# Kernel tuning notes

Hardware: AMD Instinct MI355X
Metric: run time of the kernel (lower is better)

The kernel has to match this reference:

```python
import jax, jax.numpy as jnp
import numpy as np

B, S, H, E, I, TOP_K = 2, 1024, 1024, 8, 1408, 2
W_SCALE = 0.02


def setup_inputs() -> dict:
    key = jax.random.key(0)
    ks = jax.random.split(key, 5)
    return {
        "hidden_states": jax.random.normal(ks[0], (B, S, H), dtype=jnp.float32),
        "router_weight": jax.random.normal(ks[1], (H, E), dtype=jnp.float32) * W_SCALE,
        "gate_proj": jax.random.normal(ks[2], (E, H, I), dtype=jnp.float32) * W_SCALE,
        "up_proj": jax.random.normal(ks[3], (E, H, I), dtype=jnp.float32) * W_SCALE,
        "down_proj": jax.random.normal(ks[4], (E, I, H), dtype=jnp.float32) * W_SCALE,
        "gate_bias": jnp.zeros((E, I), dtype=jnp.float32),
        "up_bias": jnp.zeros((E, I), dtype=jnp.float32),
        "down_bias": jnp.zeros((E, H), dtype=jnp.float32),
        "top_k": TOP_K,
    }


def reference(hidden_states, router_weight, gate_proj, up_proj, down_proj,
              gate_bias, up_bias, down_bias, top_k):
    b, s, h = hidden_states.shape
    e = gate_proj.shape[0]
    x = hidden_states.reshape(-1, h)              # [T, H], T = b*s
    t = x.shape[0]

    # --- RouterAdapter: MoEGate top-k then scatter into dense scores [T, E] ---
    logits = x @ router_weight                    # [T, E]
    probs = jax.nn.softmax(logits, axis=-1)
    topk_w, topk_idx = jax.lax.top_k(probs, top_k)  # [T, k]
    topk_w = topk_w / jnp.sum(topk_w, axis=-1, keepdims=True)  # norm_topk_prob
    scores = jnp.zeros((t, e), dtype=topk_w.dtype)
    scores = scores.at[jnp.arange(t)[:, None], topk_idx].set(topk_w)

    # --- StackedExperts.sparse_forward (dense equivalent of sparse matmuls) ---
    g = jnp.einsum('th,ehi->tei', x, gate_proj) + gate_bias[None]  # [T, E, I]
    u = jnp.einsum('th,ehi->tei', x, up_proj) + up_bias[None]      # [T, E, I]
    act = jax.nn.silu(g) * u                       # ACTIVATION_DEEPSEEK
    d = jnp.einsum('tei,eih->teh', act, down_proj) + down_bias[None]  # [T, E, H]

    # combine per-expert outputs with router scores (non-routed scores are 0,
    # matching the sparse matmul's zero blocks)
    y = jnp.einsum('teh,te->th', d, scores)
    return y.reshape(b, s, h)
```

## Files before the change

kernel.cpp:

```cpp
#include <hip/hip_runtime.h>

#define T_TOK 2048
#define HDIM  1024
#define NEXP  8
#define IDIM  1408

#define BM 128
#define BN 64
#define BK 32
#define KPAD 40
#define MT_SLOTS 16
#define GU_NT 22
#define DN_NT 16
#define DK_HALF 704

#define GU_BLOCKS   (8 * GU_NT * MT_SLOTS)
#define PREP_RTR    512
#define PREP_GRID   (PREP_RTR + 16 * 176)
#define GUWD_GRID   (GU_BLOCKS + 8 * 176)

typedef __attribute__((ext_vector_type(8))) short bf16x8;
typedef __attribute__((ext_vector_type(4))) float f32x4;

static __device__ __forceinline__ unsigned short f2bf(float f) {
    union { float f; unsigned u; } a; a.f = f;
    return (unsigned short)((a.u + 0x7fffu + ((a.u >> 16) & 1u)) >> 16);
}

__global__ __launch_bounds__(256) void prep_kernel(
    const float* __restrict__ x,
    const float* __restrict__ rw,
    const float* __restrict__ gw,
    const float* __restrict__ uw,
    int*   __restrict__ sel,
    float* __restrict__ w1arr,
    unsigned short* __restrict__ xb,
    unsigned short* __restrict__ gwt,
    unsigned short* __restrict__ uwt)
{
    __shared__ __align__(16) char smem[32768];
    const int tid = threadIdx.x;
    const int bx  = blockIdx.x;

    if (bx < PREP_RTR) {
        float (*rwT)[HDIM] = (float (*)[HDIM])smem;
#pragma unroll
        for (int p = 0; p < 4; ++p) {
            const int h = tid + 256 * p;
            const float4 a = *(const float4*)(rw + (size_t)h * 8);
            const float4 b = *(const float4*)(rw + (size_t)h * 8 + 4);
            rwT[0][h] = a.x; rwT[1][h] = a.y; rwT[2][h] = a.z; rwT[3][h] = a.w;
            rwT[4][h] = b.x; rwT[5][h] = b.y; rwT[6][h] = b.z; rwT[7][h] = b.w;
        }
        __syncthreads();

        const int t    = bx * 4 + (tid >> 6);
        const int lane = tid & 63;
        if (t >= T_TOK) return;

        float xr[16];
        const float* xp = x + (size_t)t * HDIM;
#pragma unroll
        for (int i = 0; i < 16; ++i) xr[i] = xp[lane + 64 * i];

        unsigned short* xbp = xb + (size_t)t * HDIM;
#pragma unroll
        for (int i = 0; i < 16; ++i) xbp[lane + 64 * i] = f2bf(xr[i]);

        double logits[NEXP];
#pragma unroll
        for (int e = 0; e < NEXP; ++e) {
            double s = 0.0;
#pragma unroll
            for (int i = 0; i < 16; ++i)
                s += (double)xr[i] * (double)rwT[e][lane + 64 * i];
#pragma unroll
            for (int off = 32; off > 0; off >>= 1)
                s += __shfl_down(s, off, 64);
            logits[e] = s;
        }

        if (lane == 0) {
            int e1 = 0;
            for (int e = 1; e < NEXP; ++e) if (logits[e] > logits[e1]) e1 = e;
            int e2 = -1;
            for (int e = 0; e < NEXP; ++e) {
                if (e == e1) continue;
                if (e2 < 0 || logits[e] > logits[e2]) e2 = e;
            }
            const double w1 = 1.0 / (1.0 + exp(logits[e2] - logits[e1]));
            sel[t]   = e1 | (e2 << 8);
            w1arr[t] = (float)w1;
        }
    } else {
        const int idx = bx - PREP_RTR;
        const int z   = idx / 176;
        const int b   = idx - z * 176;
        const int e   = z & 7;
        const float* src = (z < 8 ? gw : uw) + (size_t)e * HDIM * IDIM;
        unsigned short* dst =
            (z < 8 ? gwt : uwt) + (size_t)e * (size_t)IDIM * HDIM;
        const int nb = b % 11, kb = b / 11;
        const int k0 = kb * 64, n0 = nb * 128;

        unsigned short (*tb)[66] = (unsigned short (*)[66])smem;

        const int lk = tid >> 5;
        const int ln = (tid & 31) * 4;
#pragma unroll
        for (int r = 0; r < 8; ++r) {
            const int k = r * 8 + lk;
            const float4 v =
                *(const float4*)(src + (size_t)(k0 + k) * IDIM + n0 + ln);
            tb[ln + 0][k] = f2bf(v.x);
            tb[ln + 1][k] = f2bf(v.y);
            tb[ln + 2][k] = f2bf(v.z);
            tb[ln + 3][k] = f2bf(v.w);
        }
        __syncthreads();

        const int wn = tid >> 3;
        const int wk = (tid & 7) * 8;
#pragma unroll
        for (int p = 0; p < 4; ++p) {
            const int n = p * 32 + wn;
            const unsigned* rp = (const unsigned*)&tb[n][wk];
            uint4 o;
            o.x = rp[0]; o.y = rp[1]; o.z = rp[2]; o.w = rp[3];
            *(uint4*)(dst + (size_t)(n0 + n) * HDIM + k0 + wk) = o;
        }
    }
}

__global__ __launch_bounds__(1024) void router_scatter_kernel(
    const int* __restrict__ sel, const float* __restrict__ w1arr,
    int* __restrict__ counts,
    int* __restrict__ tok_list, float* __restrict__ wgt_list,
    int* __restrict__ row_list)
{
    __shared__ int cnt[NEXP];
    const int tid = threadIdx.x;
    if (tid < NEXP) cnt[tid] = 0;
    __syncthreads();
    for (int t = tid; t < T_TOK; t += 1024) {
        const int s  = sel[t];
        const int e1 = s & 255, e2 = s >> 8;
        const float w1 = w1arr[t];
        const int p1 = atomicAdd(&cnt[e1], 1);
        tok_list[e1 * T_TOK + p1] = t;
        wgt_list[e1 * T_TOK + p1] = w1;
        row_list[e1 * T_TOK + p1] = 2 * t;
        const int p2 = atomicAdd(&cnt[e2], 1);
        tok_list[e2 * T_TOK + p2] = t;
        wgt_list[e2 * T_TOK + p2] = 1.0f - w1;
        row_list[e2 * T_TOK + p2] = 2 * t + 1;
    }
    __syncthreads();
    if (tid < NEXP) counts[tid] = cnt[tid];
}

__global__ __launch_bounds__(256) void gateup_wd_kernel(
    const unsigned short* __restrict__ xb,
    const unsigned short* __restrict__ gwt,
    const unsigned short* __restrict__ uwt,
    const float* __restrict__ gb, const float* __restrict__ ub,
    const int* __restrict__ counts,
    const int* __restrict__ tok_list,
    const int* __restrict__ row_list,
    unsigned short* __restrict__ act,
    const float* __restrict__ dw,
    unsigned short* __restrict__ dwt)
{
    __shared__ __align__(16) char smem[21504];
    const int tid  = threadIdx.x;
    const int flat = blockIdx.x;

    if (flat >= GU_BLOCKS) {
        const int idx = flat - GU_BLOCKS;
        const int e   = idx / 176;
        const int b   = idx - e * 176;
        const float* src = dw + (size_t)e * IDIM * HDIM;
        unsigned short* dst = dwt + (size_t)e * (size_t)HDIM * IDIM;
        const int nb = b & 7, kb = b >> 3;
        const int k0 = kb * 64, n0 = nb * 128;

        unsigned short (*tb)[66] = (unsigned short (*)[66])smem;

        const int lk = tid >> 5;
        const int ln = (tid & 31) * 4;
#pragma unroll
        for (int r = 0; r < 8; ++r) {
            const int k = r * 8 + lk;
            const float4 v =
                *(const float4*)(src + (size_t)(k0 + k) * HDIM + n0 + ln);
            tb[ln + 0][k] = f2bf(v.x);
            tb[ln + 1][k] = f2bf(v.y);
            tb[ln + 2][k] = f2bf(v.z);
            tb[ln + 3][k] = f2bf(v.w);
        }
        __syncthreads();

        const int wn = tid >> 3;
        const int wk = (tid & 7) * 8;
#pragma unroll
        for (int p = 0; p < 4; ++p) {
            const int n = p * 32 + wn;
            const unsigned* rp = (const unsigned*)&tb[n][wk];
            uint4 o;
            o.x = rp[0]; o.y = rp[1]; o.z = rp[2]; o.w = rp[3];
            *(uint4*)(dst + (size_t)(n0 + n) * IDIM + k0 + wk) = o;
        }
        return;
    }

    unsigned short (*As)[KPAD] = (unsigned short (*)[KPAD])smem;
    unsigned short (*Bg)[KPAD] = (unsigned short (*)[KPAD])(smem + 10240);
    unsigned short (*Bu)[KPAD] = (unsigned short (*)[KPAD])(smem + 15360);
    int* gr_lds = (int*)(smem + 20480);
    int* or_lds = (int*)(smem + 20992);

    const int xcd  = flat & 7;
    const int q    = flat >> 3;
    const int mt   = q & 15;
    const int slot = q >> 4;
    const int P    = slot * 8 + xcd;
    const int e    = P / GU_NT;
    const int nt   = P % GU_NT;
    const int n_e  = counts[e];
    const int m0   = mt * BM;
    if (m0 >= n_e) return;
    const int n0 = nt * BN;

    const unsigned short* gwp = gwt + (size_t)e * IDIM * HDIM;
    const unsigned short* uwp = uwt + (size_t)e * IDIM * HDIM;
    const float* gbp = gb + (size_t)e * IDIM;
    const float* ubp = ub + (size_t)e * IDIM;

    const int base = e * T_TOK;
    if (tid < BM) {
        const int m = m0 + tid;
        int g = -1, o = -1;
        if (m < n_e) { g = tok_list[base + m]; o = row_list[base + m]; }
        gr_lds[tid] = g; or_lds[tid] = o;
    }
    __syncthreads();

    const int ar = tid >> 1;
    const int ac = (tid & 1) * 16;
    const int arow = gr_lds[ar];
    const unsigned short* ap = xb + (size_t)(arow < 0 ? 0 : arow) * HDIM;
    const int u   = tid & 127;
    const int brow = u >> 1;
    const int bch  = (u & 1) * 16;
    const unsigned short* bsrc =
        ((tid >> 7) ? uwp : gwp) + (size_t)(n0 + brow) * HDIM + bch;
    unsigned short* Bdst =
        ((tid >> 7) ? &Bu[0][0] : &Bg[0][0]) + brow * KPAD + bch;

    const int wv = tid >> 6, lane = tid & 63;
    const int wm = (wv & 1) * 64, wn = (wv >> 1) * 32;
    const int l16 = lane & 15, quad = lane >> 4;

    f32x4 accg[4][2], accu[4][2];
    const f32x4 zero = {0.0f, 0.0f, 0.0f, 0.0f};
#pragma unroll
    for (int i = 0; i < 4; ++i)
#pragma unroll
        for (int j = 0; j < 2; ++j) { accg[i][j] = zero; accu[i][j] = zero; }

    uint4 PA0 = {0,0,0,0}, PA1 = {0,0,0,0}, PB0, PB1;
    if (arow >= 0) {
        PA0 = *(const uint4*)(ap + ac);
        PA1 = *(const uint4*)(ap + ac + 8);
    }
    PB0 = *(const uint4*)(bsrc);
    PB1 = *(const uint4*)(bsrc + 8);

    for (int k0 = 0; k0 < HDIM; k0 += BK) {
        __syncthreads();
        *(uint4*)&As[ar][ac]       = PA0;
        *(uint4*)&As[ar][ac + 8]   = PA1;
        *(uint4*)(Bdst)            = PB0;
        *(uint4*)(Bdst + 8)        = PB1;
        __syncthreads();

        const int kn = k0 + BK;
        if (kn < HDIM) {
            if (arow >= 0) {
                PA0 = *(const uint4*)(ap + kn + ac);
                PA1 = *(const uint4*)(ap + kn + ac + 8);
            }
            PB0 = *(const uint4*)(bsrc + kn);
            PB1 = *(const uint4*)(bsrc + kn + 8);
        }

        bf16x8 af[4], bgf[2], buf_[2];
#pragma unroll
        for (int i = 0; i < 4; ++i)
            af[i] = *(const bf16x8*)&As[wm + i * 16 + l16][quad * 8];
#pragma unroll
        for (int j = 0; j < 2; ++j) {
            bgf[j]  = *(const bf16x8*)&Bg[wn + j * 16 + l16][quad * 8];
            buf_[j] = *(const bf16x8*)&Bu[wn + j * 16 + l16][quad * 8];
        }
#pragma unroll
        for (int i = 0; i < 4; ++i)
#pragma unroll
            for (int j = 0; j < 2; ++j) {
                accg[i][j] = __builtin_amdgcn_mfma_f32_16x16x32_bf16(
                    af[i], bgf[j], accg[i][j], 0, 0, 0);
                accu[i][j] = __builtin_amdgcn_mfma_f32_16x16x32_bf16(
                    af[i], buf_[j], accu[i][j], 0, 0, 0);
            }
    }

#pragma unroll
    for (int j = 0; j < 2; ++j) {
        const int nl = n0 + wn + j * 16 + l16;
        const float gbv = gbp[nl];
        const float ubv = ubp[nl];
#pragma unroll
        for (int i = 0; i < 4; ++i) {
#pragma unroll
            for (int ii = 0; ii < 4; ++ii) {
                const int ml = wm + i * 16 + quad * 4 + ii;
                const int orow = or_lds[ml];
                if (orow >= 0) {
                    const float g = accg[i][j][ii] + gbv;
                    const float uu = accu[i][j][ii] + ubv;
                    act[(size_t)orow * IDIM + nl] =
                        f2bf(g * uu / (1.0f + __expf(-g)));
                }
            }
        }
    }
}

__global__ __launch_bounds__(256) void down_kernel(
    const unsigned short* __restrict__ act,
    const unsigned short* __restrict__ dwt,
    const float* __restrict__ db,
    const int* __restrict__ counts,
    const float* __restrict__ wgt_list,
    const int* __restrict__ row_list,
    float* __restrict__ y2)
{
    const int flat = blockIdx.x;
    const int xcd  = flat & 7;
    const int q    = flat >> 3;
    const int mt   = q & 15;
    const int slot = q >> 4;
    const int P    = slot * 8 + xcd;
    const int sk   = P & 1;
    const int en   = P >> 1;
    const int e    = en >> 4;
    const int nt   = en & 15;
    const int n_e  = counts[e];
    const int m0   = mt * BM;
    if (m0 >= n_e) return;
    const int n0 = nt * BN;
    const int ks = sk * DK_HALF;
    float* y2s = y2 + (size_t)sk * 2 * T_TOK * HDIM;

    const unsigned short* dwp = dwt + (size_t)e * HDIM * IDIM;
    const float* dbp = db + (size_t)e * HDIM;

    __shared__ unsigned short As[BM][KPAD];
    __shared__ unsigned short Bs[BN][KPAD];
    __shared__ int   r_lds[BM];
    __shared__ float w_lds[BM];

    const int tid = threadIdx.x;
    const int base = e * T_TOK;
    if (tid < BM) {
        const int m = m0 + tid;
        int r = -1; float w = 0.0f;
        if (m < n_e) { r = row_list[base + m]; w = wgt_list[base + m]; }
        r_lds[tid] = r; w_lds[tid] = w;
    }
    __syncthreads();

    const int ar = tid >> 1;
    const int ac = (tid & 1) * 16;
    const int arow = r_lds[ar];
    const unsigned short* ap = act + (size_t)(arow < 0 ? 0 : arow) * IDIM + ks;
    const int brow = tid >> 2;
    const int bch  = (tid & 3) * 8;
    const unsigned short* bsrc = dwp + (size_t)(n0 + brow) * IDIM + ks + bch;
    unsigned short* Bdst = &Bs[0][0] + brow * KPAD + bch;

    const int wv = tid >> 6, lane = tid & 63;
    const int wm = (wv & 1) * 64, wn = (wv >> 1) * 32;
    const int l16 = lane & 15, quad = lane >> 4;

    f32x4 acc[4][2];
    const f32x4 zero = {0.0f, 0.0f, 0.0f, 0.0f};
#pragma unroll
    for (int i = 0; i < 4; ++i)
#pragma unroll
        for (int j = 0; j < 2; ++j) acc[i][j] = zero;

    uint4 PA0 = {0,0,0,0}, PA1 = {0,0,0,0}, PB;
    if (arow >= 0) {
        PA0 = *(const uint4*)(ap + ac);
        PA1 = *(const uint4*)(ap + ac + 8);
    }
    PB = *(const uint4*)(bsrc);

    for (int k0 = 0; k0 < DK_HALF; k0 += BK) {
        __syncthreads();
        *(uint4*)&As[ar][ac]     = PA0;
        *(uint4*)&As[ar][ac + 8] = PA1;
        *(uint4*)(Bdst)          = PB;
        __syncthreads();

        const int kn = k0 + BK;
        if (kn < DK_HALF) {
            if (arow >= 0) {
                PA0 = *(const uint4*)(ap + kn + ac);
                PA1 = *(const uint4*)(ap + kn + ac + 8);
            }
            PB = *(const uint4*)(bsrc + kn);
        }

        bf16x8 af[4], bfr[2];
#pragma unroll
        for (int i = 0; i < 4; ++i)
            af[i] = *(const bf16x8*)&As[wm + i * 16 + l16][quad * 8];
#pragma unroll
        for (int j = 0; j < 2; ++j)
            bfr[j] = *(const bf16x8*)&Bs[wn + j * 16 + l16][quad * 8];
#pragma unroll
        for (int i = 0; i < 4; ++i)
#pragma unroll
            for (int j = 0; j < 2; ++j)
                acc[i][j] = __builtin_amdgcn_mfma_f32_16x16x32_bf16(
                    af[i], bfr[j], acc[i][j], 0, 0, 0);
    }

#pragma unroll
    for (int j = 0; j < 2; ++j) {
        const int nl = n0 + wn + j * 16 + l16;
        const float bv = (sk == 0) ? dbp[nl] : 0.0f;
#pragma unroll
        for (int i = 0; i < 4; ++i) {
#pragma unroll
            for (int ii = 0; ii < 4; ++ii) {
                const int ml = wm + i * 16 + quad * 4 + ii;
                const int rr = r_lds[ml];
                if (rr >= 0)
                    y2s[(size_t)rr * HDIM + nl] = w_lds[ml] * (acc[i][j][ii] + bv);
            }
        }
    }
}

__global__ __launch_bounds__(256) void combine_kernel(
    const float* __restrict__ y2, float* __restrict__ out)
{
    const int idx = (blockIdx.x * 256 + threadIdx.x) * 4;
    const int t = idx >> 10;
    const int h = idx & 1023;
    const float* y2b = y2 + (size_t)2 * T_TOK * HDIM;
    const float4 a0 = *(const float4*)(y2  + ((size_t)2 * t) * HDIM + h);
    const float4 a1 = *(const float4*)(y2  + ((size_t)2 * t + 1) * HDIM + h);
    const float4 b0 = *(const float4*)(y2b + ((size_t)2 * t) * HDIM + h);
    const float4 b1 = *(const float4*)(y2b + ((size_t)2 * t + 1) * HDIM + h);
    float4 o;
    o.x = a0.x + a1.x + b0.x + b1.x;
    o.y = a0.y + a1.y + b0.y + b1.y;
    o.z = a0.z + a1.z + b0.z + b1.z;
    o.w = a0.w + a1.w + b0.w + b1.w;
    *(float4*)(out + idx) = o;
}

extern "C" void kernel_launch(void* const* d_in, const int* in_sizes, int n_in,
                              void* d_out, int out_size, void* d_ws, size_t ws_size,
                              hipStream_t stream)
{
    const float* x      = (const float*)d_in[0];
    const float* rw     = (const float*)d_in[1];
    const float* gate_w = (const float*)d_in[2];
    const float* up_w   = (const float*)d_in[3];
    const float* down_w = (const float*)d_in[4];
    const float* gate_b = (const float*)d_in[5];
    const float* up_b   = (const float*)d_in[6];
    const float* down_b = (const float*)d_in[7];
    float* out = (float*)d_out;

    char* ws = (char*)d_ws;
    size_t off = 0;
    int*   counts   = (int*)(ws + off);  off += 256;
    int*   tok_list = (int*)(ws + off);  off += 65536;
    float* wgt_list = (float*)(ws + off); off += 65536;
    int*   row_list = (int*)(ws + off);  off += 65536;
    int*   sel      = (int*)(ws + off);  off += T_TOK * 4;
    float* w1arr    = (float*)(ws + off); off += T_TOK * 4;
    unsigned short* x_bf = (unsigned short*)(ws + off); off += (size_t)T_TOK * HDIM * 2;
    unsigned short* act  = (unsigned short*)(ws + off); off += (size_t)2 * T_TOK * IDIM * 2;
    unsigned short* dwt  = (unsigned short*)(ws + off); off += (size_t)NEXP * IDIM * HDIM * 2;
    unsigned short* gwt  = (unsigned short*)(ws + off); off += (size_t)NEXP * IDIM * HDIM * 2;
    unsigned short* uwt  = (unsigned short*)(ws + off);
    float* y2 = (float*)gwt;

    prep_kernel<<<PREP_GRID, 256, 0, stream>>>(
        x, rw, gate_w, up_w, sel, w1arr, x_bf, gwt, uwt);

    router_scatter_kernel<<<1, 1024, 0, stream>>>(
        sel, w1arr, counts, tok_list, wgt_list, row_list);

    gateup_wd_kernel<<<GUWD_GRID, 256, 0, stream>>>(
        x_bf, gwt, uwt, gate_b, up_b, counts, tok_list, row_list, act,
        down_w, dwt);

    down_kernel<<<2 * 8 * DN_NT * MT_SLOTS, 256, 0, stream>>>(
        act, dwt, down_b, counts, wgt_list, row_list, y2);

    combine_kernel<<<(T_TOK * HDIM / 4) / 256, 256, 0, stream>>>(y2, out);
}
```

Measured before the change: 277.5 us.

## Load GEMM tiles directly into LDS with global_load_lds, dropping register prefetch

Both the gate/up and down-projection GEMM loops now use the global_load_lds builtin to copy 16-byte chunks straight from global memory into shared memory, instead of staging them through registers. The LDS rows lose their padding (32 instead of 40 shorts) to match the contiguous per-wave layout that direct loads write. This removes register staging and the VGPR-to-LDS stores, and the smaller footprint may allow higher occupancy. In exchange the register-level prefetch of the next tile is gone, so load latency is no longer overlapped with MFMA work. The unpadded rows may also cause LDS bank conflicts on fragment reads, and padding rows (negative indices) now load token 0's data instead of zeros.

```diff
diff --git a/kernel.cpp b/kernel.cpp
--- a/kernel.cpp
+++ b/kernel.cpp
@@ -8,7 +8,6 @@
 #define BM 128
 #define BN 64
 #define BK 32
-#define KPAD 40
 #define MT_SLOTS 16
 #define GU_NT 22
 #define DN_NT 16
@@ -19,6 +18,13 @@
 #define PREP_GRID   (PREP_RTR + 16 * 176)
 #define GUWD_GRID   (GU_BLOCKS + 8 * 176)
 
+#define SM_A    0
+#define SM_G    8192
+#define SM_U    12288
+#define SM_GR   16384
+#define SM_OR   16896
+#define SM_SZ   17408
+
 typedef __attribute__((ext_vector_type(8))) short bf16x8;
 typedef __attribute__((ext_vector_type(4))) float f32x4;
 
@@ -26,6 +32,11 @@
     union { float f; unsigned u; } a; a.f = f;
     return (unsigned short)((a.u + 0x7fffu + ((a.u >> 16) & 1u)) >> 16);
 }
+
+#define GLOAD16(gsrc, ldst)                                                  \
+    __builtin_amdgcn_global_load_lds(                                        \
+        (const __attribute__((address_space(1))) unsigned int*)(gsrc),       \
+        (__attribute__((address_space(3))) unsigned int*)(ldst), 16, 0, 0)
 
 __global__ __launch_bounds__(256) void prep_kernel(
     const float* __restrict__ x,
@@ -171,7 +182,7 @@
     const float* __restrict__ dw,
     unsigned short* __restrict__ dwt)
 {
-    __shared__ __align__(16) char smem[21504];
+    __shared__ __align__(16) char smem[SM_SZ];
     const int tid  = threadIdx.x;
     const int flat = blockIdx.x;
 
@@ -213,11 +224,11 @@
         return;
     }
 
-    unsigned short (*As)[KPAD] = (unsigned short (*)[KPAD])smem;
-    unsigned short (*Bg)[KPAD] = (unsigned short (*)[KPAD])(smem + 10240);
-    unsigned short (*Bu)[KPAD] = (unsigned short (*)[KPAD])(smem + 15360);
-    int* gr_lds = (int*)(smem + 20480);
-    int* or_lds = (int*)(smem + 20992);
+    unsigned short (*As)[32] = (unsigned short (*)[32])(smem + SM_A);
+    unsigned short (*Bg)[32] = (unsigned short (*)[32])(smem + SM_G);
+    unsigned short (*Bu)[32] = (unsigned short (*)[32])(smem + SM_U);
+    int* gr_lds = (int*)(smem + SM_GR);
+    int* or_lds = (int*)(smem + SM_OR);
 
     const int xcd  = flat & 7;
     const int q    = flat >> 3;
@@ -245,19 +256,23 @@
     }
     __syncthreads();
 
-    const int ar = tid >> 1;
-    const int ac = (tid & 1) * 16;
-    const int arow = gr_lds[ar];
-    const unsigned short* ap = xb + (size_t)(arow < 0 ? 0 : arow) * HDIM;
-    const int u   = tid & 127;
-    const int brow = u >> 1;
-    const int bch  = (u & 1) * 16;
-    const unsigned short* bsrc =
-        ((tid >> 7) ? uwp : gwp) + (size_t)(n0 + brow) * HDIM + bch;
-    unsigned short* Bdst =
-        ((tid >> 7) ? &Bu[0][0] : &Bg[0][0]) + brow * KPAD + bch;
-
     const int wv = tid >> 6, lane = tid & 63;
+    const int lr = lane >> 2;
+    const int lc = (lane & 3) * 8;
+
+    const int r0 = 32 * wv + lr;
+    const int r1 = 32 * wv + 16 + lr;
+    int a0 = gr_lds[r0]; if (a0 < 0) a0 = 0;
+    int a1 = gr_lds[r1]; if (a1 < 0) a1 = 0;
+    const unsigned short* apA0 = xb + (size_t)a0 * HDIM + lc;
+    const unsigned short* apA1 = xb + (size_t)a1 * HDIM + lc;
+    unsigned short* dA0 = &As[32 * wv][0];
+    unsigned short* dA1 = &As[32 * wv + 16][0];
+    const unsigned short* gpB = gwp + (size_t)(n0 + 16 * wv + lr) * HDIM + lc;
+    const unsigned short* upB = uwp + (size_t)(n0 + 16 * wv + lr) * HDIM + lc;
+    unsigned short* dBg = &Bg[16 * wv][0];
+    unsigned short* dBu = &Bu[16 * wv][0];
+
     const int wm = (wv & 1) * 64, wn = (wv >> 1) * 32;
     const int l16 = lane & 15, quad = lane >> 4;
 
@@ -268,31 +283,13 @@
 #pragma unroll
         for (int j = 0; j < 2; ++j) { accg[i][j] = zero; accu[i][j] = zero; }
 
-    uint4 PA0 = {0,0,0,0}, PA1 = {0,0,0,0}, PB0, PB1;
-    if (arow >= 0) {
-        PA0 = *(const uint4*)(ap + ac);
-        PA1 = *(const uint4*)(ap + ac + 8);
-    }
-    PB0 = *(const uint4*)(bsrc);
-    PB1 = *(const uint4*)(bsrc + 8);
-
     for (int k0 = 0; k0 < HDIM; k0 += BK) {
         __syncthreads();
-        *(uint4*)&As[ar][ac]       = PA0;
-        *(uint4*)&As[ar][ac + 8]   = PA1;
-        *(uint4*)(Bdst)            = PB0;
-        *(uint4*)(Bdst + 8)        = PB1;
-        __syncthreads();
-
-        const int kn = k0 + BK;
-        if (kn < HDIM) {
-            if (arow >= 0) {
-                PA0 = *(const uint4*)(ap + kn + ac);
-                PA1 = *(const uint4*)(ap + kn + ac + 8);
-            }
-            PB0 = *(const uint4*)(bsrc + kn);
-            PB1 = *(const uint4*)(bsrc + kn + 8);
-        }
+        GLOAD16(apA0 + k0, dA0);
+        GLOAD16(apA1 + k0, dA1);
+        GLOAD16(gpB + k0, dBg);
+        GLOAD16(upB + k0, dBu);
+        __syncthreads();
 
         bf16x8 af[4], bgf[2], buf_[2];
 #pragma unroll
@@ -365,8 +362,8 @@
     const unsigned short* dwp = dwt + (size_t)e * HDIM * IDIM;
     const float* dbp = db + (size_t)e * HDIM;
 
-    __shared__ unsigned short As[BM][KPAD];
-    __shared__ unsigned short Bs[BN][KPAD];
+    __shared__ unsigned short As[BM][32];
+    __shared__ unsigned short Bs[BN][32];
     __shared__ int   r_lds[BM];
     __shared__ float w_lds[BM];
 
@@ -380,16 +377,22 @@
     }
     __syncthreads();
 
-    const int ar = tid >> 1;
-    const int ac = (tid & 1) * 16;
-    const int arow = r_lds[ar];
-    const unsigned short* ap = act + (size_t)(arow < 0 ? 0 : arow) * IDIM + ks;
-    const int brow = tid >> 2;
-    const int bch  = (tid & 3) * 8;
-    const unsigned short* bsrc = dwp + (size_t)(n0 + brow) * IDIM + ks + bch;
-    unsigned short* Bdst = &Bs[0][0] + brow * KPAD + bch;
-
     const int wv = tid >> 6, lane = tid & 63;
+    const int lr = lane >> 2;
+    const int lc = (lane & 3) * 8;
+
+    const int r0 = 32 * wv + lr;
+    const int r1 = 32 * wv + 16 + lr;
+    int a0 = r_lds[r0]; if (a0 < 0) a0 = 0;
+    int a1 = r_lds[r1]; if (a1 < 0) a1 = 0;
+    const unsigned short* apA0 = act + (size_t)a0 * IDIM + ks + lc;
+    const unsigned short* apA1 = act + (size_t)a1 * IDIM + ks + lc;
+    unsigned short* dA0 = &As[32 * wv][0];
+    unsigned short* dA1 = &As[32 * wv + 16][0];
+    const unsigned short* bpB =
+        dwp + (size_t)(n0 + 16 * wv + lr) * IDIM + ks + lc;
+    unsigned short* dB = &Bs[16 * wv][0];
+
     const int wm = (wv & 1) * 64, wn = (wv >> 1) * 32;
     const int l16 = lane & 15, quad = lane >> 4;
 
@@ -400,28 +403,12 @@
 #pragma unroll
         for (int j = 0; j < 2; ++j) acc[i][j] = zero;
 
-    uint4 PA0 = {0,0,0,0}, PA1 = {0,0,0,0}, PB;
-    if (arow >= 0) {
-        PA0 = *(const uint4*)(ap + ac);
-        PA1 = *(const uint4*)(ap + ac + 8);
-    }
-    PB = *(const uint4*)(bsrc);
-
     for (int k0 = 0; k0 < DK_HALF; k0 += BK) {
         __syncthreads();
-        *(uint4*)&As[ar][ac]     = PA0;
-        *(uint4*)&As[ar][ac + 8] = PA1;
-        *(uint4*)(Bdst)          = PB;
-        __syncthreads();
-
-        const int kn = k0 + BK;
-        if (kn < DK_HALF) {
-            if (arow >= 0) {
-                PA0 = *(const uint4*)(ap + kn + ac);
-                PA1 = *(const uint4*)(ap + kn + ac + 8);
-            }
-            PB = *(const uint4*)(bsrc + kn);
-        }
+        GLOAD16(apA0 + k0, dA0);
+        GLOAD16(apA1 + k0, dA1);
+        GLOAD16(bpB + k0, dB);
+        __syncthreads();
 
         bf16x8 af[4], bfr[2];
 #pragma unroll
```

Result: no change. 273.4 us (-1.5%).
